# Kernel tuning notes

Hardware: AMD Instinct MI355X
Metric: run time of the kernel (lower is better)

Reference implementation:

```python
import jax, jax.numpy as jnp
import numpy as np

N_NODES = 50000
N_EDGES = 800000
D = 128
N_LAYERS = 3
EPS = 1e-5  # torch LayerNorm default


def _gcn_conv(x, src, dst, dinv, W, b):
    # PyG GCNConv: h = x @ W; out[i] = sum_{(s->i)} dinv[s]*dinv[i]*h[s] + dinv[i]^2*h[i] + b
    h = x @ W
    norm = dinv[src] * dinv[dst]                      # [E]
    msgs = h[src] * norm[:, None]                     # [E, D] gather
    agg = jax.ops.segment_sum(msgs, dst, num_segments=N_NODES)  # scatter-add
    agg = agg + h * (dinv * dinv)[:, None]            # self-loop term
    return agg + b


def _layer_norm(x, gamma, beta):
    mu = jnp.mean(x, axis=-1, keepdims=True)
    var = jnp.mean(jnp.square(x - mu), axis=-1, keepdims=True)
    return (x - mu) * jax.lax.rsqrt(var + EPS) * gamma + beta


def setup_inputs() -> dict:
    key = jax.random.key(0)
    ks = jax.random.split(key, 4)
    x = jax.random.normal(ks[0], (N_NODES, D), dtype=jnp.float32)
    edge_index = jax.random.randint(ks[1], (2, N_EDGES), 0, N_NODES, dtype=jnp.int64)
    Ws = jax.random.normal(ks[2], (N_LAYERS, D, D), dtype=jnp.float32) * (1.0 / np.sqrt(D))
    bs = jnp.zeros((N_LAYERS, D), dtype=jnp.float32)
    gammas = jnp.ones((N_LAYERS, D), dtype=jnp.float32)
    betas = jnp.zeros((N_LAYERS, D), dtype=jnp.float32)
    return {"x": x, "edge_index": edge_index, "Ws": Ws, "bs": bs,
            "gammas": gammas, "betas": betas}


def reference(x, edge_index, Ws, bs, gammas, betas):
    src, dst = edge_index[0], edge_index[1]
    # GCN symmetric normalization with self-loops: deg[i] = in-degree(i) + 1
    deg = jnp.zeros((N_NODES,), dtype=x.dtype).at[dst].add(1.0) + 1.0
    dinv = jax.lax.rsqrt(deg)
    h = x
    for i in range(N_LAYERS):
        x_new = _gcn_conv(h, src, dst, dinv, Ws[i], bs[i])
        x_new = _layer_norm(x_new, gammas[i], betas[i])
        x_new = jax.nn.relu(x_new)  # dropout is identity in eval mode
        h = h + x_new if i > 0 else x_new
    return h
```

## Files before the change

### kernel.cpp

```cpp
#include <hip/hip_runtime.h>
#include <hip/hip_bf16.h>

#define NN 50000
#define NE 800000
#define DD 128
#define NB 196
#define NCH 8
#define CHSZ 6250
#define NC2 (NN * NCH)
#define NSB 391
#define PH (64 * NB)
#define FS 2048
#define NSL 391
#define HB 3125
#define CB 3125
#define WB 192
#define LN_EPS 1e-5f

typedef __bf16 bf16x8 __attribute__((ext_vector_type(8)));
typedef float f32x4 __attribute__((ext_vector_type(4)));

__device__ inline ushort f2bf_bits(float f) {
    union { __hip_bfloat16 h; ushort u; } c;
    c.h = __float2bfloat16(f);
    return c.u;
}

__global__ void hist_cast_kernel(const int* __restrict__ src, const int* __restrict__ dst,
                                 int* __restrict__ counts2, const float* __restrict__ x,
                                 uint4* __restrict__ fb0, const float* __restrict__ W,
                                 ushort* __restrict__ Wt) {
    int b = blockIdx.x;
    if (b < HB) {
        int e = b * 256 + threadIdx.x;
        int s = src[e], d = dst[e];
        atomicAdd(&counts2[d * NCH + s / CHSZ], 1);
    } else if (b < HB + CB) {
        int i = (b - HB) * 256 + threadIdx.x;
        float4 v0 = ((const float4*)x)[2 * i];
        float4 v1 = ((const float4*)x)[2 * i + 1];
        union { ushort us[8]; uint4 u; } pk;
        pk.us[0] = f2bf_bits(v0.x); pk.us[1] = f2bf_bits(v0.y);
        pk.us[2] = f2bf_bits(v0.z); pk.us[3] = f2bf_bits(v0.w);
        pk.us[4] = f2bf_bits(v1.x); pk.us[5] = f2bf_bits(v1.y);
        pk.us[6] = f2bf_bits(v1.z); pk.us[7] = f2bf_bits(v1.w);
        fb0[i] = pk.u;
    } else {
        int i = (b - HB - CB) * 256 + threadIdx.x;
        int l = i >> 14, k = (i >> 7) & 127, n = i & 127;
        Wt[l * 16384 + n * 128 + k] = f2bf_bits(W[i]);
    }
}

__global__ __launch_bounds__(1024) void scan1024_blocks(int* __restrict__ data,
                                                        int* __restrict__ bsums) {
    __shared__ int ws[16];
    int gid = blockIdx.x * 1024 + threadIdx.x;
    int lane = threadIdx.x & 63, wid = threadIdx.x >> 6;
    int v = (gid < NC2) ? data[gid] : 0;
    int x = v;
#pragma unroll
    for (int off = 1; off < 64; off <<= 1) {
        int t = __shfl_up(x, off, 64);
        if (lane >= off) x += t;
    }
    if (lane == 63) ws[wid] = x;
    __syncthreads();
    if (threadIdx.x == 0) {
        int run = 0;
        for (int i = 0; i < 16; ++i) { int t = ws[i]; ws[i] = run; run += t; }
        bsums[blockIdx.x] = run;
    }
    __syncthreads();
    if (gid < NC2) data[gid] = x - v + ws[wid];
}

__global__ __launch_bounds__(1024) void scan_sums1024(int* __restrict__ bsums, int nb) {
    __shared__ int ws[16];
    int tid = threadIdx.x;
    int lane = tid & 63, wid = tid >> 6;
    int v = (tid < nb) ? bsums[tid] : 0;
    int x = v;
#pragma unroll
    for (int off = 1; off < 64; off <<= 1) {
        int t = __shfl_up(x, off, 64);
        if (lane >= off) x += t;
    }
    if (lane == 63) ws[wid] = x;
    __syncthreads();
    if (tid == 0) {
        int run = 0;
        for (int i = 0; i < 16; ++i) { int t = ws[i]; ws[i] = run; run += t; }
    }
    __syncthreads();
    if (tid < nb) bsums[tid] = x - v + ws[wid];
}

__global__ void finalize_kernel(const int* __restrict__ excl2, const int* __restrict__ bsums,
                                int* __restrict__ row_ptr, int* __restrict__ next_pos2,
                                float* __restrict__ dinv, int* __restrict__ degarr,
                                int* __restrict__ bh) {
    __shared__ int lh[64];
    if (threadIdx.x < 64) lh[threadIdx.x] = 0;
    __syncthreads();
    int d = blockIdx.x * 256 + threadIdx.x;
    if (d < NN) {
        int base = d * NCH;
        int p0 = excl2[base] + bsums[base >> 10];
#pragma unroll
        for (int c = 0; c < NCH; ++c) {
            int idx = base + c;
            next_pos2[idx] = excl2[idx] + bsums[idx >> 10];
        }
        int nxt = (d == NN - 1) ? NE : excl2[base + NCH] + bsums[(base + NCH) >> 10];
        int deg = nxt - p0;
        row_ptr[d] = p0;
        dinv[d] = rsqrtf((float)deg + 1.0f);
        degarr[d] = deg;
        atomicAdd(&lh[min(deg, 63)], 1);
    }
    __syncthreads();
    if (threadIdx.x < 64) bh[threadIdx.x * NB + blockIdx.x] = lh[threadIdx.x];
    if (blockIdx.x == 0 && threadIdx.x == 0) row_ptr[NN] = NE;
}

__global__ __launch_bounds__(1024) void permscan_kernel(int* __restrict__ bh) {
    __shared__ int wsum[16];
    const int CH = 13;
    int tid = threadIdx.x;
    int base = tid * CH;
    int vals[CH];
    int s = 0;
#pragma unroll
    for (int i = 0; i < CH; ++i) {
        int idx = base + i;
        int v = (idx < PH) ? bh[idx] : 0;
        vals[i] = s;
        s += v;
    }
    int lane = tid & 63, wid = tid >> 6;
    int x = s;
#pragma unroll
    for (int off = 1; off < 64; off <<= 1) {
        int t = __shfl_up(x, off, 64);
        if (lane >= off) x += t;
    }
    if (lane == 63) wsum[wid] = x;
    __syncthreads();
    if (tid == 0) {
        int run = 0;
        for (int i = 0; i < 16; ++i) { int t = wsum[i]; wsum[i] = run; run += t; }
    }
    __syncthreads();
    int texcl = x - s + wsum[wid];
#pragma unroll
    for (int i = 0; i < CH; ++i) {
        int idx = base + i;
        if (idx < PH) bh[idx] = texcl + vals[i];
    }
}

__global__ void permscatter_kernel(const int* __restrict__ degarr, const int* __restrict__ bh,
                                   int* __restrict__ perm) {
    __shared__ int lh[64];
    __shared__ int lbase[64];
    if (threadIdx.x < 64) {
        lh[threadIdx.x] = 0;
        lbase[threadIdx.x] = bh[threadIdx.x * NB + blockIdx.x];
    }
    __syncthreads();
    int gid = blockIdx.x * 256 + threadIdx.x;
    if (gid < NN) {
        int b = min(degarr[gid], 63);
        int r = atomicAdd(&lh[b], 1);
        perm[lbase[b] + r] = gid;
    }
}

__global__ void fill_kernel(const int* __restrict__ src, const int* __restrict__ dst,
                            int* __restrict__ next_pos2, const float* __restrict__ dinv,
                            int2* __restrict__ edge2) {
    int slice = blockIdx.x >> 3;
    int r = blockIdx.x & 7;
    int base = slice * FS;
#pragma unroll 2
    for (int i = threadIdx.x; i < FS; i += 256) {
        int e = base + i;
        if (e < NE) {
            int d = dst[e];
            if (d / CHSZ == r) {
                int s = src[e];
                int pos = atomicAdd(&next_pos2[d * NCH + s / CHSZ], 1);
                int2 o;
                o.x = s;
                o.y = __float_as_int(dinv[s] * dinv[d]);
                edge2[pos] = o;
            }
        }
    }
}

template <bool RES, bool FINAL>
__global__ __launch_bounds__(256) void layer_kernel(
    const ushort* __restrict__ fin, const int* __restrict__ row_ptr,
    const int2* __restrict__ edge2, const int* __restrict__ perm,
    const float* __restrict__ dinv, const ushort* __restrict__ Wt,
    const float* __restrict__ bias, const float* __restrict__ gamma,
    const float* __restrict__ beta, ushort* __restrict__ fout, float* __restrict__ out) {
    __shared__ uint4 sA[16 * 17];
    __shared__ int sNode[16];
    __shared__ float sLN1[4][16], sLN2[4][16];

    int w = threadIdx.x >> 6, lane = threadIdx.x & 63;
    int g = lane >> 4, t = lane & 15;
    int arow = w * 4 + g;
    int slot = blockIdx.x * 16 + arow;
    int node = perm[slot];
    if (t == 0) sNode[arow] = node;

    {
        int beg = row_ptr[node], end = row_ptr[node + 1];
        const uint4* cu4 = (const uint4*)fin;
        float acc[8] = {};
        int e = beg;
        for (; e + 8 <= end; e += 8) {
            int2 a[8];
            uint4 v[8];
#pragma unroll
            for (int j = 0; j < 8; ++j) a[j] = edge2[e + j];
#pragma unroll
            for (int j = 0; j < 8; ++j) v[j] = cu4[a[j].x * 16 + t];
#pragma unroll
            for (int j = 0; j < 8; ++j) {
                uint vv[4] = {v[j].x, v[j].y, v[j].z, v[j].w};
                float ww = __int_as_float(a[j].y);
#pragma unroll
                for (int i = 0; i < 4; ++i) {
                    acc[2 * i] = fmaf(ww, __uint_as_float(vv[i] << 16), acc[2 * i]);
                    acc[2 * i + 1] =
                        fmaf(ww, __uint_as_float(vv[i] & 0xffff0000u), acc[2 * i + 1]);
                }
            }
        }
        for (; e + 4 <= end; e += 4) {
            int2 a[4];
            uint4 v[4];
#pragma unroll
            for (int j = 0; j < 4; ++j) a[j] = edge2[e + j];
#pragma unroll
            for (int j = 0; j < 4; ++j) v[j] = cu4[a[j].x * 16 + t];
#pragma unroll
            for (int j = 0; j < 4; ++j) {
                uint vv[4] = {v[j].x, v[j].y, v[j].z, v[j].w};
                float ww = __int_as_float(a[j].y);
#pragma unroll
                for (int i = 0; i < 4; ++i) {
                    acc[2 * i] = fmaf(ww, __uint_as_float(vv[i] << 16), acc[2 * i]);
                    acc[2 * i + 1] =
                        fmaf(ww, __uint_as_float(vv[i] & 0xffff0000u), acc[2 * i + 1]);
                }
            }
        }
        for (; e < end; ++e) {
            int2 a = edge2[e];
            uint4 v = cu4[a.x * 16 + t];
            uint vv[4] = {v.x, v.y, v.z, v.w};
            float ww = __int_as_float(a.y);
#pragma unroll
            for (int i = 0; i < 4; ++i) {
                acc[2 * i] = fmaf(ww, __uint_as_float(vv[i] << 16), acc[2 * i]);
                acc[2 * i + 1] = fmaf(ww, __uint_as_float(vv[i] & 0xffff0000u), acc[2 * i + 1]);
            }
        }
        float di = dinv[node];
        float w2s = di * di;
        {
            uint4 v = cu4[node * 16 + t];
            uint vv[4] = {v.x, v.y, v.z, v.w};
#pragma unroll
            for (int i = 0; i < 4; ++i) {
                acc[2 * i] = fmaf(w2s, __uint_as_float(vv[i] << 16), acc[2 * i]);
                acc[2 * i + 1] = fmaf(w2s, __uint_as_float(vv[i] & 0xffff0000u), acc[2 * i + 1]);
            }
        }
        union { ushort us[8]; uint4 u; } pk;
#pragma unroll
        for (int i = 0; i < 8; ++i) pk.us[i] = f2bf_bits(acc[i]);
        sA[arow * 17 + t] = pk.u;
    }
    __syncthreads();

    int q = lane >> 4, m = lane & 15;
    f32x4 c0 = (f32x4){0.f, 0.f, 0.f, 0.f};
    f32x4 c1 = (f32x4){0.f, 0.f, 0.f, 0.f};
    int n0 = 16 * (2 * w), n1 = 16 * (2 * w + 1);
#pragma unroll
    for (int kk = 0; kk < 4; ++kk) {
        bf16x8 af = *(const bf16x8*)&sA[m * 17 + kk * 4 + q];
        bf16x8 b0 = *(const bf16x8*)(Wt + (n0 + m) * DD + kk * 32 + q * 8);
        bf16x8 b1 = *(const bf16x8*)(Wt + (n1 + m) * DD + kk * 32 + q * 8);
        c0 = __builtin_amdgcn_mfma_f32_16x16x32_bf16(af, b0, c0, 0, 0, 0);
        c1 = __builtin_amdgcn_mfma_f32_16x16x32_bf16(af, b1, c1, 0, 0, 0);
    }

    float bb0 = bias[n0 + m], bb1 = bias[n1 + m];
    float s1[4], s2[4];
#pragma unroll
    for (int r = 0; r < 4; ++r) {
        float v0 = c0[r] + bb0, v1 = c1[r] + bb1;
        c0[r] = v0; c1[r] = v1;
        s1[r] = v0 + v1;
        s2[r] = v0 * v0 + v1 * v1;
    }
#pragma unroll
    for (int off = 1; off <= 8; off <<= 1) {
#pragma unroll
        for (int r = 0; r < 4; ++r) {
            s1[r] += __shfl_xor(s1[r], off, 64);
            s2[r] += __shfl_xor(s2[r], off, 64);
        }
    }
    if (m == 0) {
#pragma unroll
        for (int r = 0; r < 4; ++r) {
            sLN1[w][q * 4 + r] = s1[r];
            sLN2[w][q * 4 + r] = s2[r];
        }
    }
    __syncthreads();
    float ga0 = gamma[n0 + m], ga1 = gamma[n1 + m];
    float be0 = beta[n0 + m], be1 = beta[n1 + m];
#pragma unroll
    for (int r = 0; r < 4; ++r) {
        int row = q * 4 + r;
        float S1 = sLN1[0][row] + sLN1[1][row] + sLN1[2][row] + sLN1[3][row];
        float S2 = sLN2[0][row] + sLN2[1][row] + sLN2[2][row] + sLN2[3][row];
        float mu = S1 * (1.f / 128.f);
        float var = S2 * (1.f / 128.f) - mu * mu;
        float rstd = rsqrtf(var + LN_EPS);
        int nd = sNode[row];
        size_t rb = (size_t)nd * DD;
        float o0 = fmaxf((c0[r] - mu) * rstd * ga0 + be0, 0.f);
        float o1 = fmaxf((c1[r] - mu) * rstd * ga1 + be1, 0.f);
        if (RES) {
            o0 += __uint_as_float(((uint)fin[rb + n0 + m]) << 16);
            o1 += __uint_as_float(((uint)fin[rb + n1 + m]) << 16);
        }
        if (FINAL) {
            out[rb + n0 + m] = o0;
            out[rb + n1 + m] = o1;
        } else {
            fout[rb + n0 + m] = f2bf_bits(o0);
            fout[rb + n1 + m] = f2bf_bits(o1);
        }
    }
}


extern "C" void kernel_launch(void* const* d_in, const int* in_sizes, int n_in,
                              void* d_out, int out_size, void* d_ws, size_t ws_size,
                              hipStream_t stream) {
    const float* x = (const float*)d_in[0];
    const int* edge = (const int*)d_in[1];
    const float* Ws = (const float*)d_in[2];
    const float* bs = (const float*)d_in[3];
    const float* gs = (const float*)d_in[4];
    const float* bes = (const float*)d_in[5];
    float* out = (float*)d_out;
    const int* src = edge;
    const int* dst = edge + NE;

    char* p = (char*)d_ws;
    int* counts2 = (int*)p;     p += (size_t)NC2 * 4;
    int* bsums = (int*)p;       p += 1024 * 4;
    int* row_ptr = (int*)p;     p += (size_t)(NN + 4) * 4;
    int* next_pos2 = (int*)p;   p += (size_t)NC2 * 4;
    float* dinv = (float*)p;    p += (size_t)NN * 4;
    int* degarr = (int*)p;      p += (size_t)NN * 4;
    int* bh = (int*)p;          p += (size_t)PH * 4;
    int* perm = (int*)p;        p += (size_t)NN * 4;
    int2* edge2 = (int2*)p;     p += (size_t)NE * 8;
    ushort* fb0 = (ushort*)p;   p += (size_t)NN * DD * 2;
    ushort* fb1 = (ushort*)p;   p += (size_t)NN * DD * 2;
    ushort* Wt = (ushort*)p;    p += (size_t)3 * DD * DD * 2;

    hipMemsetAsync(counts2, 0, (size_t)NC2 * 4, stream);
    hist_cast_kernel<<<HB + CB + WB, 256, 0, stream>>>(src, dst, counts2, x, (uint4*)fb0, Ws,
                                                       Wt);
    scan1024_blocks<<<NSB, 1024, 0, stream>>>(counts2, bsums);
    scan_sums1024<<<1, 1024, 0, stream>>>(bsums, NSB);
    finalize_kernel<<<NB, 256, 0, stream>>>(counts2, bsums, row_ptr, next_pos2, dinv, degarr,
                                            bh);
    permscan_kernel<<<1, 1024, 0, stream>>>(bh);
    permscatter_kernel<<<NB, 256, 0, stream>>>(degarr, bh, perm);
    fill_kernel<<<NSL * 8, 256, 0, stream>>>(src, dst, next_pos2, dinv, edge2);

    int lg = NN / 16;
    layer_kernel<false, false><<<lg, 256, 0, stream>>>(
        fb0, row_ptr, edge2, perm, dinv, Wt, bs, gs, bes, fb1, out);
    layer_kernel<true, false><<<lg, 256, 0, stream>>>(
        fb1, row_ptr, edge2, perm, dinv, Wt + 16384, bs + DD, gs + DD, bes + DD, fb0, out);
    layer_kernel<true, true><<<lg, 256, 0, stream>>>(
        fb0, row_ptr, edge2, perm, dinv, Wt + 32768, bs + 2 * DD, gs + 2 * DD, bes + 2 * DD,
        fb1, out);
}
```

Measured before the change: 330.8 us.

## Merge permscatter and fill kernels, add nontemporal edge loads and output stores

Merges the perm scatter and the edge fill into a single launch, with block index choosing the role, which removes one kernel launch boundary. In the aggregation loop it drops the 8-edge unrolled stage, processing edges 4 at a time as 64-bit nontemporal loads. Output feature stores become nontemporal. The nontemporal hints try to keep streaming data from evicting gathered features in cache, but the smaller unroll gives fewer gathers in flight per step. Nontemporal stores of the bf16 buffers, which the next layer reads back, may also lose cache reuse.

```diff
diff --git a/kernel.cpp b/kernel.cpp
--- a/kernel.cpp
+++ b/kernel.cpp
@@ -160,41 +160,42 @@
     }
 }
 
-__global__ void permscatter_kernel(const int* __restrict__ degarr, const int* __restrict__ bh,
-                                   int* __restrict__ perm) {
-    __shared__ int lh[64];
-    __shared__ int lbase[64];
-    if (threadIdx.x < 64) {
-        lh[threadIdx.x] = 0;
-        lbase[threadIdx.x] = bh[threadIdx.x * NB + blockIdx.x];
-    }
-    __syncthreads();
-    int gid = blockIdx.x * 256 + threadIdx.x;
-    if (gid < NN) {
-        int b = min(degarr[gid], 63);
-        int r = atomicAdd(&lh[b], 1);
-        perm[lbase[b] + r] = gid;
-    }
-}
-
-__global__ void fill_kernel(const int* __restrict__ src, const int* __restrict__ dst,
-                            int* __restrict__ next_pos2, const float* __restrict__ dinv,
-                            int2* __restrict__ edge2) {
-    int slice = blockIdx.x >> 3;
-    int r = blockIdx.x & 7;
-    int base = slice * FS;
+__global__ void scatter_fill_kernel(const int* __restrict__ degarr, const int* __restrict__ bh,
+                                    int* __restrict__ perm, const int* __restrict__ src,
+                                    const int* __restrict__ dst, int* __restrict__ next_pos2,
+                                    const float* __restrict__ dinv, int2* __restrict__ edge2) {
+    if (blockIdx.x < NB) {
+        __shared__ int lh[64];
+        __shared__ int lbase[64];
+        if (threadIdx.x < 64) {
+            lh[threadIdx.x] = 0;
+            lbase[threadIdx.x] = bh[threadIdx.x * NB + blockIdx.x];
+        }
+        __syncthreads();
+        int gid = blockIdx.x * 256 + threadIdx.x;
+        if (gid < NN) {
+            int b = min(degarr[gid], 63);
+            int r = atomicAdd(&lh[b], 1);
+            perm[lbase[b] + r] = gid;
+        }
+    } else {
+        int bb = blockIdx.x - NB;
+        int slice = bb >> 3;
+        int r = bb & 7;
+        int base = slice * FS;
 #pragma unroll 2
-    for (int i = threadIdx.x; i < FS; i += 256) {
-        int e = base + i;
-        if (e < NE) {
-            int d = dst[e];
-            if (d / CHSZ == r) {
-                int s = src[e];
-                int pos = atomicAdd(&next_pos2[d * NCH + s / CHSZ], 1);
-                int2 o;
-                o.x = s;
-                o.y = __float_as_int(dinv[s] * dinv[d]);
-                edge2[pos] = o;
+        for (int i = threadIdx.x; i < FS; i += 256) {
+            int e = base + i;
+            if (e < NE) {
+                int d = dst[e];
+                if (d / CHSZ == r) {
+                    int s = src[e];
+                    int pos = atomicAdd(&next_pos2[d * NCH + s / CHSZ], 1);
+                    int2 o;
+                    o.x = s;
+                    o.y = __float_as_int(dinv[s] * dinv[d]);
+                    edge2[pos] = o;
+                }
             }
         }
     }
@@ -221,19 +222,20 @@
     {
         int beg = row_ptr[node], end = row_ptr[node + 1];
         const uint4* cu4 = (const uint4*)fin;
+        const long long* e8 = (const long long*)edge2;
         float acc[8] = {};
         int e = beg;
-        for (; e + 8 <= end; e += 8) {
-            int2 a[8];
-            uint4 v[8];
-#pragma unroll
-            for (int j = 0; j < 8; ++j) a[j] = edge2[e + j];
-#pragma unroll
-            for (int j = 0; j < 8; ++j) v[j] = cu4[a[j].x * 16 + t];
-#pragma unroll
-            for (int j = 0; j < 8; ++j) {
+        for (; e + 4 <= end; e += 4) {
+            long long a[4];
+            uint4 v[4];
+#pragma unroll
+            for (int j = 0; j < 4; ++j) a[j] = __builtin_nontemporal_load(&e8[e + j]);
+#pragma unroll
+            for (int j = 0; j < 4; ++j) v[j] = cu4[((int)a[j]) * 16 + t];
+#pragma unroll
+            for (int j = 0; j < 4; ++j) {
                 uint vv[4] = {v[j].x, v[j].y, v[j].z, v[j].w};
-                float ww = __int_as_float(a[j].y);
+                float ww = __int_as_float((int)(a[j] >> 32));
 #pragma unroll
                 for (int i = 0; i < 4; ++i) {
                     acc[2 * i] = fmaf(ww, __uint_as_float(vv[i] << 16), acc[2 * i]);
@@ -242,30 +244,11 @@
                 }
             }
         }
-        for (; e + 4 <= end; e += 4) {
-            int2 a[4];
-            uint4 v[4];
-#pragma unroll
-            for (int j = 0; j < 4; ++j) a[j] = edge2[e + j];
-#pragma unroll
-            for (int j = 0; j < 4; ++j) v[j] = cu4[a[j].x * 16 + t];
-#pragma unroll
-            for (int j = 0; j < 4; ++j) {
-                uint vv[4] = {v[j].x, v[j].y, v[j].z, v[j].w};
-                float ww = __int_as_float(a[j].y);
-#pragma unroll
-                for (int i = 0; i < 4; ++i) {
-                    acc[2 * i] = fmaf(ww, __uint_as_float(vv[i] << 16), acc[2 * i]);
-                    acc[2 * i + 1] =
-                        fmaf(ww, __uint_as_float(vv[i] & 0xffff0000u), acc[2 * i + 1]);
-                }
-            }
-        }
         for (; e < end; ++e) {
-            int2 a = edge2[e];
-            uint4 v = cu4[a.x * 16 + t];
+            long long a = __builtin_nontemporal_load(&e8[e]);
+            uint4 v = cu4[((int)a) * 16 + t];
             uint vv[4] = {v.x, v.y, v.z, v.w};
-            float ww = __int_as_float(a.y);
+            float ww = __int_as_float((int)(a >> 32));
 #pragma unroll
             for (int i = 0; i < 4; ++i) {
                 acc[2 * i] = fmaf(ww, __uint_as_float(vv[i] << 16), acc[2 * i]);
@@ -347,11 +330,11 @@
             o1 += __uint_as_float(((uint)fin[rb + n1 + m]) << 16);
         }
         if (FINAL) {
-            out[rb + n0 + m] = o0;
-            out[rb + n1 + m] = o1;
+            __builtin_nontemporal_store(o0, &out[rb + n0 + m]);
+            __builtin_nontemporal_store(o1, &out[rb + n1 + m]);
         } else {
-            fout[rb + n0 + m] = f2bf_bits(o0);
-            fout[rb + n1 + m] = f2bf_bits(o1);
+            __builtin_nontemporal_store(f2bf_bits(o0), &fout[rb + n0 + m]);
+            __builtin_nontemporal_store(f2bf_bits(o1), &fout[rb + n1 + m]);
         }
     }
 }
@@ -392,8 +375,8 @@
     finalize_kernel<<<NB, 256, 0, stream>>>(counts2, bsums, row_ptr, next_pos2, dinv, degarr,
                                             bh);
     permscan_kernel<<<1, 1024, 0, stream>>>(bh);
-    permscatter_kernel<<<NB, 256, 0, stream>>>(degarr, bh, perm);
-    fill_kernel<<<NSL * 8, 256, 0, stream>>>(src, dst, next_pos2, dinv, edge2);
+    scatter_fill_kernel<<<NB + NSL * 8, 256, 0, stream>>>(degarr, bh, perm, src, dst,
+                                                          next_pos2, dinv, edge2);
 
     int lg = NN / 16;
     layer_kernel<false, false><<<lg, 256, 0, stream>>>(
```

Measured after the change: 331.6 us. No clear change (+0.2%).
